# Performance work log

Hardware: AMD Instinct MI355X
Metric: run time of the kernel (lower is better)

Reference implementation:

```python
import jax, jax.numpy as jnp
import numpy as np

MAX_P = 20
MAX_N = 50
FDIM = 256
SCALE = 0.08
STEPS = 3


def _grid_sample_border(feat_hwc, grid):
    # feat_hwc: [B,H,W,C]; grid: [B,Q,2] normalized xy in [-1,1]
    # Bilinear grid_sample, padding_mode='border', align_corners=False (matches torch).
    B, H, W, C = feat_hwc.shape

    def one(fm, g):  # fm [H,W,C], g [Q,2]
        ix = jnp.clip(((g[:, 0] + 1.0) * W - 1.0) * 0.5, 0.0, W - 1.0)
        iy = jnp.clip(((g[:, 1] + 1.0) * H - 1.0) * 0.5, 0.0, H - 1.0)
        x0f = jnp.floor(ix); y0f = jnp.floor(iy)
        wx = (ix - x0f)[:, None]; wy = (iy - y0f)[:, None]
        x0 = x0f.astype(jnp.int32); y0 = y0f.astype(jnp.int32)
        x1 = jnp.minimum(x0 + 1, W - 1); y1 = jnp.minimum(y0 + 1, H - 1)
        f00 = fm[y0, x0]; f01 = fm[y0, x1]  # [Q,C]
        f10 = fm[y1, x0]; f11 = fm[y1, x1]
        top = f00 * (1.0 - wx) + f01 * wx
        bot = f10 * (1.0 - wx) + f11 * wx
        return top * (1.0 - wy) + bot * wy

    return jax.vmap(one)(feat_hwc, grid)


def setup_inputs() -> dict:
    key = jax.random.key(0)
    ks = jax.random.split(key, 12)
    d = {
        'p2': jax.random.normal(ks[0], (4, 256, 256, 256), jnp.float32),
        'p4': jax.random.normal(ks[1], (4, 256, 64, 64), jnp.float32),
        'iw1': jax.random.normal(ks[2], (16384, 512), jnp.float32) * 0.01,
        'ib1': jnp.zeros((512,), jnp.float32),
        'iw2': jax.random.normal(ks[3], (512, 1024), jnp.float32) * 0.04,
        'ib2': jnp.zeros((1024,), jnp.float32),
        'iw3': jax.random.normal(ks[4], (1024, 2000), jnp.float32) * 0.03,
        'ib3': jnp.zeros((2000,), jnp.float32),
        'rw1': jax.random.normal(ks[5], (258, 256), jnp.float32) * 0.06,
        'rb1': jnp.zeros((256,), jnp.float32),
        'rw2': jax.random.normal(ks[6], (256, 128), jnp.float32) * 0.06,
        'rb2': jnp.zeros((128,), jnp.float32),
        'rw3': jax.random.normal(ks[7], (128, 2), jnp.float32) * 0.09,
        'rb3': jnp.zeros((2,), jnp.float32),
        'vw1': jax.random.normal(ks[8], (100, 128), jnp.float32) * 0.1,
        'vb1': jnp.zeros((128,), jnp.float32),
        'vw2': jax.random.normal(ks[9], (128, 1), jnp.float32) * 0.09,
        'vb2': jnp.zeros((1,), jnp.float32),
    }
    return d


def reference(p2, p4, iw1, ib1, iw2, ib2, iw3, ib3,
              rw1, rb1, rw2, rb2, rw3, rb3, vw1, vb1, vw2, vb2):
    B = p4.shape[0]
    # AdaptiveAvgPool2d(8) on 64x64 -> mean over 8x8 blocks
    pooled = p4.reshape(B, FDIM, 8, 8, 8, 8).mean(axis=(3, 5))  # [B,C,8,8]
    flat = pooled.reshape(B, -1)  # [B, C*64]
    h = jax.nn.relu(flat @ iw1 + ib1)
    h = jax.nn.relu(h @ iw2 + ib2)
    init_polygons = jax.nn.sigmoid(h @ iw3 + ib3).reshape(B, MAX_P, MAX_N, 2)

    feat_hwc = jnp.transpose(p2, (0, 2, 3, 1))  # [B,H,W,C]
    polygons = init_polygons
    for _ in range(STEPS):
        coords = polygons.reshape(B, -1, 2)           # [B,Q,2] in [0,1]
        grid = coords * 2.0 - 1.0
        sampled = _grid_sample_border(feat_hwc, grid)  # [B,Q,C]
        inp = jnp.concatenate([sampled, coords], axis=-1)  # [B,Q,C+2]
        r = jax.nn.relu(inp @ rw1 + rb1)
        r = jax.nn.relu(r @ rw2 + rb2)
        disp = jnp.tanh(r @ rw3 + rb3).reshape(B, MAX_P, MAX_N, 2)
        bad = ~jnp.all(jnp.isfinite(disp))
        disp = jnp.where(bad, 0.0,
                         jnp.clip(disp * SCALE, -2.0 * SCALE, 2.0 * SCALE))
        polygons = jnp.clip(polygons + disp, 0.0, 1.0)

    poly_flat = polygons.reshape(B * MAX_P, MAX_N * 2)
    v = jax.nn.relu(poly_flat @ vw1 + vb1)
    validity = jax.nn.sigmoid(v @ vw2 + vb2).reshape(B, MAX_P)
    return polygons, validity, init_polygons
```

## Files before the change

### kernel.cpp

```cpp
#include <hip/hip_runtime.h>
#include <hip/hip_fp16.h>
#include <math.h>

#define WS_FLAT 0
#define WS_PART 65536
#define WS_H1   (65536 + 524288)
#define WS_H2   (WS_H1 + 2048)
#define WS_POLY (WS_H2 + 4096)
#define WS_P2T  1048576

__global__ void __launch_bounds__(256) transpose_k(const float* __restrict__ in,
                                                   __half* __restrict__ out) {
    __shared__ float t[64][65];
    int tile = blockIdx.x;
    int b  = tile >> 12;
    int ct = (tile >> 10) & 3;
    int xt = tile & 1023;
    int c0 = ct << 6, yx0 = xt << 6;
    int tid = threadIdx.x;

    int jv = (tid & 15) << 2;
    int i0 = tid >> 4;
    const float* ip = in + (((size_t)(b * 256 + c0)) << 16) + yx0;
    #pragma unroll
    for (int ii = i0; ii < 64; ii += 16) {
        float4 v = *(const float4*)(ip + ((size_t)ii << 16) + jv);
        t[jv + 0][ii] = v.x; t[jv + 1][ii] = v.y;
        t[jv + 2][ii] = v.z; t[jv + 3][ii] = v.w;
    }
    __syncthreads();

    int cl = (tid & 7) << 3;
    #pragma unroll
    for (int jj = tid >> 3; jj < 64; jj += 32) {
        union { __half h[8]; float4 f; } u;
        #pragma unroll
        for (int q = 0; q < 8; ++q) u.h[q] = __float2half(t[jj][cl + q]);
        *(float4*)(out + ((size_t)b << 24) + ((size_t)(yx0 + jj) << 8) + c0 + cl) = u.f;
    }
}

__global__ void pool_k(const float* __restrict__ p4, float* __restrict__ flat) {
    int o = blockIdx.x * blockDim.x + threadIdx.x;
    int b = o >> 14;
    int c = (o >> 6) & 255;
    int ij = o & 63;
    int i = ij >> 3, j = ij & 7;
    const float* base = p4 + (((size_t)(b * 256 + c) * 64 + i * 8) * 64 + j * 8);
    float s = 0.f;
    #pragma unroll
    for (int u = 0; u < 8; ++u) {
        const float4* r = (const float4*)(base + u * 64);
        float4 a = r[0], bb = r[1];
        s += a.x + a.y + a.z + a.w + bb.x + bb.y + bb.z + bb.w;
    }
    flat[o] = s * (1.0f / 64.0f);
}

__global__ void g1a_k(const float* __restrict__ flat, const float* __restrict__ iw1,
                      float* __restrict__ part) {
    __shared__ float sf[4][64];
    int tid = threadIdx.x;
    int kbase = blockIdx.x * 64;
    if (tid < 256) sf[tid >> 6][tid & 63] = flat[(tid >> 6) * 16384 + kbase + (tid & 63)];
    __syncthreads();
    float a0 = 0.f, a1 = 0.f, a2 = 0.f, a3 = 0.f;
    for (int k = 0; k < 64; ++k) {
        float w = iw1[(size_t)(kbase + k) * 512 + tid];
        a0 = fmaf(sf[0][k], w, a0);
        a1 = fmaf(sf[1][k], w, a1);
        a2 = fmaf(sf[2][k], w, a2);
        a3 = fmaf(sf[3][k], w, a3);
    }
    float* pp = part + (size_t)blockIdx.x * 2048;
    pp[tid] = a0; pp[512 + tid] = a1; pp[1024 + tid] = a2; pp[1536 + tid] = a3;
}

__global__ void g1b_k(const float* __restrict__ part, const float* __restrict__ ib1,
                      float* __restrict__ h1) {
    __shared__ float red[8][32];
    int tid = threadIdx.x;
    int cc = tid >> 5, oo = tid & 31;
    int o = blockIdx.x * 32 + oo;
    float s = 0.f;
    for (int i = 0; i < 32; ++i)
        s += part[(size_t)(cc + 8 * i) * 2048 + o];
    red[cc][oo] = s;
    __syncthreads();
    if (cc == 0) {
        float t = 0.f;
        #pragma unroll
        for (int c2 = 0; c2 < 8; ++c2) t += red[c2][oo];
        t += ib1[o & 511];
        h1[o] = fmaxf(t, 0.f);
    }
}

__global__ void g2_k(const float* __restrict__ h1, const float* __restrict__ iw2,
                     const float* __restrict__ ib2, float* __restrict__ h2) {
    __shared__ float sh[512];
    __shared__ float red[4][64];
    int tid = threadIdx.x;
    int b = blockIdx.x >> 4, jt = blockIdx.x & 15;
    sh[tid] = h1[b * 512 + tid];
    sh[tid + 256] = h1[b * 512 + 256 + tid];
    __syncthreads();
    int j = (jt << 6) + (tid & 63);
    int kc = tid >> 6;
    float acc = 0.f;
    for (int k = kc * 128; k < kc * 128 + 128; ++k)
        acc = fmaf(sh[k], iw2[(size_t)k * 1024 + j], acc);
    red[kc][tid & 63] = acc;
    __syncthreads();
    if (kc == 0) {
        float t = red[0][tid] + red[1][tid] + red[2][tid] + red[3][tid] + ib2[j];
        h2[b * 1024 + j] = fmaxf(t, 0.f);
    }
}

__global__ void g3_k(const float* __restrict__ h2, const float* __restrict__ iw3,
                     const float* __restrict__ ib3, float* __restrict__ out_init,
                     float* __restrict__ poly) {
    __shared__ float sh[1024];
    __shared__ float red[4][64];
    int tid = threadIdx.x;
    int b = blockIdx.x >> 5, jt = blockIdx.x & 31;
    const float* h = h2 + b * 1024;
    sh[tid] = h[tid]; sh[tid + 256] = h[tid + 256];
    sh[tid + 512] = h[tid + 512]; sh[tid + 768] = h[tid + 768];
    __syncthreads();
    int j = (jt << 6) + (tid & 63);
    int kc = tid >> 6;
    float acc = 0.f;
    if (j < 2000) {
        for (int k = kc * 256; k < kc * 256 + 256; ++k)
            acc = fmaf(sh[k], iw3[(size_t)k * 2000 + j], acc);
    }
    red[kc][tid & 63] = acc;
    __syncthreads();
    if (kc == 0 && j < 2000) {
        float t = red[0][tid] + red[1][tid] + red[2][tid] + red[3][tid] + ib3[j];
        float s = 1.f / (1.f + expf(-t));
        int o = b * 2000 + j;
        out_init[o] = s;
        poly[o] = s;
    }
}

__global__ void __launch_bounds__(256) step_k(
    const __half* __restrict__ p2th,
    const float* __restrict__ rw1, const float* __restrict__ rb1,
    const float* __restrict__ rw2, const float* __restrict__ rb2,
    const float* __restrict__ rw3, const float* __restrict__ rb3,
    float* __restrict__ poly) {
    __shared__ __align__(16) float s_inp[258 * 16];
    __shared__ __align__(16) float s_r1[256 * 16];
    __shared__ __align__(16) float s_r2[128 * 16];
    int tid = threadIdx.x;
    int pt0 = blockIdx.x * 16;

    {
        int ch2 = (tid & 127) << 1;
        int pgg = tid >> 7;
        float v0[8], v1[8];
        #pragma unroll
        for (int pp = 0; pp < 8; ++pp) {
            int pt = pt0 + pgg * 8 + pp;
            int b = pt / 1000;
            float cx = poly[pt * 2], cy = poly[pt * 2 + 1];
            float ix = fminf(fmaxf(cx * 256.f - 0.5f, 0.f), 255.f);
            float iy = fminf(fmaxf(cy * 256.f - 0.5f, 0.f), 255.f);
            float x0f = floorf(ix), y0f = floorf(iy);
            int x0 = (int)x0f, y0 = (int)y0f;
            int x1 = min(x0 + 1, 255), y1 = min(y0 + 1, 255);
            float wx = ix - x0f, wy = iy - y0f;
            const __half* bt = p2th + ((size_t)b << 24);
            int r0 = (y0 << 16) + (x0 << 8) + ch2;
            int r1a = (y1 << 16) + (x0 << 8) + ch2;
            int dx = (x1 - x0) << 8;
            float2 f00 = __half22float2(*(const __half2*)(bt + r0));
            float2 f01 = __half22float2(*(const __half2*)(bt + r0 + dx));
            float2 f10 = __half22float2(*(const __half2*)(bt + r1a));
            float2 f11 = __half22float2(*(const __half2*)(bt + r1a + dx));
            float t0 = f00.x + (f01.x - f00.x) * wx;
            float b0 = f10.x + (f11.x - f10.x) * wx;
            float t1 = f00.y + (f01.y - f00.y) * wx;
            float b1 = f10.y + (f11.y - f10.y) * wx;
            v0[pp] = t0 + (b0 - t0) * wy;
            v1[pp] = t1 + (b1 - t1) * wy;
        }
        float* r0p = &s_inp[ch2 * 16 + pgg * 8];
        float* r1p = &s_inp[(ch2 + 1) * 16 + pgg * 8];
        ((float4*)r0p)[0] = make_float4(v0[0], v0[1], v0[2], v0[3]);
        ((float4*)r0p)[1] = make_float4(v0[4], v0[5], v0[6], v0[7]);
        ((float4*)r1p)[0] = make_float4(v1[0], v1[1], v1[2], v1[3]);
        ((float4*)r1p)[1] = make_float4(v1[4], v1[5], v1[6], v1[7]);
        if (tid < 32) {
            int p = tid >> 1, d = tid & 1;
            s_inp[(256 + d) * 16 + p] = poly[(pt0 + p) * 2 + d];
        }
    }
    __syncthreads();

    int jc = tid & 63, pg = tid >> 6;
    {
        float4 bias = *(const float4*)(rb1 + jc * 4);
        float4 acc0 = bias, acc1 = bias, acc2 = bias, acc3 = bias;
        for (int k = 0; k < 258; ++k) {
            float4 a = *(const float4*)&s_inp[k * 16 + pg * 4];
            float4 w = *(const float4*)(rw1 + k * 256 + jc * 4);
            acc0.x = fmaf(a.x, w.x, acc0.x); acc0.y = fmaf(a.x, w.y, acc0.y);
            acc0.z = fmaf(a.x, w.z, acc0.z); acc0.w = fmaf(a.x, w.w, acc0.w);
            acc1.x = fmaf(a.y, w.x, acc1.x); acc1.y = fmaf(a.y, w.y, acc1.y);
            acc1.z = fmaf(a.y, w.z, acc1.z); acc1.w = fmaf(a.y, w.w, acc1.w);
            acc2.x = fmaf(a.z, w.x, acc2.x); acc2.y = fmaf(a.z, w.y, acc2.y);
            acc2.z = fmaf(a.z, w.z, acc2.z); acc2.w = fmaf(a.z, w.w, acc2.w);
            acc3.x = fmaf(a.w, w.x, acc3.x); acc3.y = fmaf(a.w, w.y, acc3.y);
            acc3.z = fmaf(a.w, w.z, acc3.z); acc3.w = fmaf(a.w, w.w, acc3.w);
        }
        acc0.x = fmaxf(acc0.x, 0.f); acc0.y = fmaxf(acc0.y, 0.f);
        acc0.z = fmaxf(acc0.z, 0.f); acc0.w = fmaxf(acc0.w, 0.f);
        acc1.x = fmaxf(acc1.x, 0.f); acc1.y = fmaxf(acc1.y, 0.f);
        acc1.z = fmaxf(acc1.z, 0.f); acc1.w = fmaxf(acc1.w, 0.f);
        acc2.x = fmaxf(acc2.x, 0.f); acc2.y = fmaxf(acc2.y, 0.f);
        acc2.z = fmaxf(acc2.z, 0.f); acc2.w = fmaxf(acc2.w, 0.f);
        acc3.x = fmaxf(acc3.x, 0.f); acc3.y = fmaxf(acc3.y, 0.f);
        acc3.z = fmaxf(acc3.z, 0.f); acc3.w = fmaxf(acc3.w, 0.f);
        *(float4*)&s_r1[(jc * 4 + 0) * 16 + pg * 4] = make_float4(acc0.x, acc1.x, acc2.x, acc3.x);
        *(float4*)&s_r1[(jc * 4 + 1) * 16 + pg * 4] = make_float4(acc0.y, acc1.y, acc2.y, acc3.y);
        *(float4*)&s_r1[(jc * 4 + 2) * 16 + pg * 4] = make_float4(acc0.z, acc1.z, acc2.z, acc3.z);
        *(float4*)&s_r1[(jc * 4 + 3) * 16 + pg * 4] = make_float4(acc0.w, acc1.w, acc2.w, acc3.w);
    }
    __syncthreads();

    {
        float2 bias = *(const float2*)(rb2 + jc * 2);
        float2 d0 = bias, d1 = bias, d2 = bias, d3 = bias;
        for (int k = 0; k < 256; ++k) {
            float4 a = *(const float4*)&s_r1[k * 16 + pg * 4];
            float2 w = *(const float2*)(rw2 + k * 128 + jc * 2);
            d0.x = fmaf(a.x, w.x, d0.x); d0.y = fmaf(a.x, w.y, d0.y);
            d1.x = fmaf(a.y, w.x, d1.x); d1.y = fmaf(a.y, w.y, d1.y);
            d2.x = fmaf(a.z, w.x, d2.x); d2.y = fmaf(a.z, w.y, d2.y);
            d3.x = fmaf(a.w, w.x, d3.x); d3.y = fmaf(a.w, w.y, d3.y);
        }
        d0.x = fmaxf(d0.x, 0.f); d0.y = fmaxf(d0.y, 0.f);
        d1.x = fmaxf(d1.x, 0.f); d1.y = fmaxf(d1.y, 0.f);
        d2.x = fmaxf(d2.x, 0.f); d2.y = fmaxf(d2.y, 0.f);
        d3.x = fmaxf(d3.x, 0.f); d3.y = fmaxf(d3.y, 0.f);
        *(float4*)&s_r2[(jc * 2 + 0) * 16 + pg * 4] = make_float4(d0.x, d1.x, d2.x, d3.x);
        *(float4*)&s_r2[(jc * 2 + 1) * 16 + pg * 4] = make_float4(d0.y, d1.y, d2.y, d3.y);
    }
    __syncthreads();

    if (tid < 32) {
        int p = tid >> 1, d = tid & 1;
        float acc = rb3[d];
        for (int k = 0; k < 128; ++k)
            acc = fmaf(s_r2[k * 16 + p], rw3[k * 2 + d], acc);
        float disp = tanhf(acc) * 0.08f;
        disp = fminf(fmaxf(disp, -0.16f), 0.16f);
        int idx = (pt0 + p) * 2 + d;
        float nv = poly[idx] + disp;
        poly[idx] = fminf(fmaxf(nv, 0.f), 1.f);
    }
}

__global__ void valid_k(const float* __restrict__ poly,
                        const float* __restrict__ vw1, const float* __restrict__ vb1,
                        const float* __restrict__ vw2, const float* __restrict__ vb2,
                        float* __restrict__ out) {
    __shared__ float sp[100];
    __shared__ float sred[2];
    int tid = threadIdx.x;
    int row = blockIdx.x;
    if (tid < 100) {
        float v = poly[row * 100 + tid];
        sp[tid] = v;
        out[row * 100 + tid] = v;
    }
    __syncthreads();
    float acc = vb1[tid];
    for (int k = 0; k < 100; ++k)
        acc = fmaf(sp[k], vw1[k * 128 + tid], acc);
    float pr = fmaxf(acc, 0.f) * vw2[tid];
    #pragma unroll
    for (int off = 32; off > 0; off >>= 1)
        pr += __shfl_down(pr, off, 64);
    if ((tid & 63) == 0) sred[tid >> 6] = pr;
    __syncthreads();
    if (tid == 0) {
        float s = sred[0] + sred[1] + vb2[0];
        out[8000 + row] = 1.f / (1.f + expf(-s));
    }
}

extern "C" void kernel_launch(void* const* d_in, const int* in_sizes, int n_in,
                              void* d_out, int out_size, void* d_ws, size_t ws_size,
                              hipStream_t stream) {
    const float* p2  = (const float*)d_in[0];
    const float* p4  = (const float*)d_in[1];
    const float* iw1 = (const float*)d_in[2];
    const float* ib1 = (const float*)d_in[3];
    const float* iw2 = (const float*)d_in[4];
    const float* ib2 = (const float*)d_in[5];
    const float* iw3 = (const float*)d_in[6];
    const float* ib3 = (const float*)d_in[7];
    const float* rw1 = (const float*)d_in[8];
    const float* rb1 = (const float*)d_in[9];
    const float* rw2 = (const float*)d_in[10];
    const float* rb2 = (const float*)d_in[11];
    const float* rw3 = (const float*)d_in[12];
    const float* rb3 = (const float*)d_in[13];
    const float* vw1 = (const float*)d_in[14];
    const float* vb1 = (const float*)d_in[15];
    const float* vw2 = (const float*)d_in[16];
    const float* vb2 = (const float*)d_in[17];
    float* out = (float*)d_out;
    float* ws = (float*)d_ws;
    float* flat = ws + WS_FLAT;
    float* part = ws + WS_PART;
    float* h1   = ws + WS_H1;
    float* h2   = ws + WS_H2;
    float* poly = ws + WS_POLY;
    __half* p2th = (__half*)(ws + WS_P2T);

    pool_k<<<256, 256, 0, stream>>>(p4, flat);
    g1a_k<<<256, 512, 0, stream>>>(flat, iw1, part);
    g1b_k<<<64, 256, 0, stream>>>(part, ib1, h1);
    g2_k<<<64, 256, 0, stream>>>(h1, iw2, ib2, h2);
    g3_k<<<128, 256, 0, stream>>>(h2, iw3, ib3, out + 8080, poly);
    transpose_k<<<16384, 256, 0, stream>>>(p2, p2th);
    for (int s = 0; s < 3; ++s)
        step_k<<<250, 256, 0, stream>>>(p2th, rw1, rb1, rw2, rb2, rw3, rb3, poly);
    valid_k<<<80, 128, 0, stream>>>(poly, vw1, vb1, vw2, vb2, out);
}
```

Baseline: 584.1 us.

## Fuse pooling, first GEMV and p2 transpose into one kernel; halve step block size

Merges the p4 pooling into the first MLP partial-GEMV kernel, and packs that with the p2 NCHW→NHWC fp16 transpose into a single 512-thread launch partitioned by block index. This removes launches and lets the small MLP work overlap the bandwidth-bound transpose. The refine step kernel now handles 8 points per block instead of 16, giving 500 blocks for better CU coverage. In exchange each block re-reads the weights per point pair, so weight traffic doubles, and shared memory moves to a row-major layout.

Result: slower. 599.2 us (+2.6%).

```diff
diff --git a/kernel.cpp b/kernel.cpp
--- a/kernel.cpp
+++ b/kernel.cpp
@@ -9,71 +9,64 @@
 #define WS_POLY (WS_H2 + 4096)
 #define WS_P2T  1048576
 
-__global__ void __launch_bounds__(256) transpose_k(const float* __restrict__ in,
-                                                   __half* __restrict__ out) {
-    __shared__ float t[64][65];
-    int tile = blockIdx.x;
-    int b  = tile >> 12;
-    int ct = (tile >> 10) & 3;
-    int xt = tile & 1023;
-    int c0 = ct << 6, yx0 = xt << 6;
-    int tid = threadIdx.x;
-
-    int jv = (tid & 15) << 2;
-    int i0 = tid >> 4;
-    const float* ip = in + (((size_t)(b * 256 + c0)) << 16) + yx0;
-    #pragma unroll
-    for (int ii = i0; ii < 64; ii += 16) {
-        float4 v = *(const float4*)(ip + ((size_t)ii << 16) + jv);
-        t[jv + 0][ii] = v.x; t[jv + 1][ii] = v.y;
-        t[jv + 2][ii] = v.z; t[jv + 3][ii] = v.w;
-    }
-    __syncthreads();
-
-    int cl = (tid & 7) << 3;
-    #pragma unroll
-    for (int jj = tid >> 3; jj < 64; jj += 32) {
+__global__ void __launch_bounds__(512) fused_tp_g1a(
+    const float* __restrict__ p2, __half* __restrict__ p2th,
+    const float* __restrict__ p4, const float* __restrict__ iw1,
+    float* __restrict__ part) {
+    __shared__ float smem[64 * 65];
+    int tid = threadIdx.x;
+
+    if (blockIdx.x < 256) {
+        int kb = blockIdx.x;
+        float* sf = smem;
+        if (tid < 256) {
+            int b = tid >> 6, ij = tid & 63;
+            const float* base = p4 + (((size_t)(b * 256 + kb) * 64 + (ij >> 3) * 8) * 64 + (ij & 7) * 8);
+            float s = 0.f;
+            #pragma unroll
+            for (int u = 0; u < 8; ++u) {
+                const float4* r = (const float4*)(base + u * 64);
+                float4 a = r[0], bb = r[1];
+                s += a.x + a.y + a.z + a.w + bb.x + bb.y + bb.z + bb.w;
+            }
+            sf[tid] = s * (1.0f / 64.0f);
+        }
+        __syncthreads();
+        float a0 = 0.f, a1 = 0.f, a2 = 0.f, a3 = 0.f;
+        int kbase = kb << 6;
+        for (int k = 0; k < 64; ++k) {
+            float w = iw1[(size_t)(kbase + k) * 512 + tid];
+            a0 = fmaf(sf[k],       w, a0);
+            a1 = fmaf(sf[64 + k],  w, a1);
+            a2 = fmaf(sf[128 + k], w, a2);
+            a3 = fmaf(sf[192 + k], w, a3);
+        }
+        float* pp = part + (size_t)kb * 2048;
+        pp[tid] = a0; pp[512 + tid] = a1; pp[1024 + tid] = a2; pp[1536 + tid] = a3;
+    } else {
+        int tile = blockIdx.x - 256;
+        int b  = tile >> 12;
+        int ct = (tile >> 10) & 3;
+        int xt = tile & 1023;
+        int c0 = ct << 6, yx0 = xt << 6;
+        float (*t)[65] = (float (*)[65])smem;
+
+        int jv = (tid & 15) << 2;
+        const float* ip = p2 + (((size_t)(b * 256 + c0)) << 16) + yx0;
+        #pragma unroll
+        for (int ii = tid >> 4; ii < 64; ii += 32) {
+            float4 v = *(const float4*)(ip + ((size_t)ii << 16) + jv);
+            t[jv + 0][ii] = v.x; t[jv + 1][ii] = v.y;
+            t[jv + 2][ii] = v.z; t[jv + 3][ii] = v.w;
+        }
+        __syncthreads();
+        int cl = (tid & 7) << 3;
+        int jj = tid >> 3;
         union { __half h[8]; float4 f; } u;
         #pragma unroll
         for (int q = 0; q < 8; ++q) u.h[q] = __float2half(t[jj][cl + q]);
-        *(float4*)(out + ((size_t)b << 24) + ((size_t)(yx0 + jj) << 8) + c0 + cl) = u.f;
-    }
-}
-
-__global__ void pool_k(const float* __restrict__ p4, float* __restrict__ flat) {
-    int o = blockIdx.x * blockDim.x + threadIdx.x;
-    int b = o >> 14;
-    int c = (o >> 6) & 255;
-    int ij = o & 63;
-    int i = ij >> 3, j = ij & 7;
-    const float* base = p4 + (((size_t)(b * 256 + c) * 64 + i * 8) * 64 + j * 8);
-    float s = 0.f;
-    #pragma unroll
-    for (int u = 0; u < 8; ++u) {
-        const float4* r = (const float4*)(base + u * 64);
-        float4 a = r[0], bb = r[1];
-        s += a.x + a.y + a.z + a.w + bb.x + bb.y + bb.z + bb.w;
-    }
-    flat[o] = s * (1.0f / 64.0f);
-}
-
-__global__ void g1a_k(const float* __restrict__ flat, const float* __restrict__ iw1,
-                      float* __restrict__ part) {
-    __shared__ float sf[4][64];
-    int tid = threadIdx.x;
-    int kbase = blockIdx.x * 64;
-    if (tid < 256) sf[tid >> 6][tid & 63] = flat[(tid >> 6) * 16384 + kbase + (tid & 63)];
-    __syncthreads();
-    float a0 = 0.f, a1 = 0.f, a2 = 0.f, a3 = 0.f;
-    for (int k = 0; k < 64; ++k) {
-        float w = iw1[(size_t)(kbase + k) * 512 + tid];
-        a0 = fmaf(sf[0][k], w, a0);
-        a1 = fmaf(sf[1][k], w, a1);
-        a2 = fmaf(sf[2][k], w, a2);
-        a3 = fmaf(sf[3][k], w, a3);
-    }
-    float* pp = part + (size_t)blockIdx.x * 2048;
-    pp[tid] = a0; pp[512 + tid] = a1; pp[1024 + tid] = a2; pp[1536 + tid] = a3;
+        *(float4*)(p2th + ((size_t)b << 24) + ((size_t)(yx0 + jj) << 8) + c0 + cl) = u.f;
+    }
 }
 
 __global__ void g1b_k(const float* __restrict__ part, const float* __restrict__ ib1,
@@ -153,23 +146,23 @@
     const float* __restrict__ rw2, const float* __restrict__ rb2,
     const float* __restrict__ rw3, const float* __restrict__ rb3,
     float* __restrict__ poly) {
-    __shared__ __align__(16) float s_inp[258 * 16];
-    __shared__ __align__(16) float s_r1[256 * 16];
-    __shared__ __align__(16) float s_r2[128 * 16];
-    int tid = threadIdx.x;
-    int pt0 = blockIdx.x * 16;
+    __shared__ __align__(16) float s_inp[8][258];
+    __shared__ __align__(16) float s_r1[8][256];
+    __shared__ __align__(16) float s_r2[8][130];
+    int tid = threadIdx.x;
+    int pt0 = blockIdx.x * 8;
 
     {
         int ch2 = (tid & 127) << 1;
         int pgg = tid >> 7;
-        float v0[8], v1[8];
         #pragma unroll
-        for (int pp = 0; pp < 8; ++pp) {
-            int pt = pt0 + pgg * 8 + pp;
+        for (int pp = 0; pp < 4; ++pp) {
+            int lp = pgg * 4 + pp;
+            int pt = pt0 + lp;
             int b = pt / 1000;
-            float cx = poly[pt * 2], cy = poly[pt * 2 + 1];
-            float ix = fminf(fmaxf(cx * 256.f - 0.5f, 0.f), 255.f);
-            float iy = fminf(fmaxf(cy * 256.f - 0.5f, 0.f), 255.f);
+            float2 cxy = *(const float2*)(poly + pt * 2);
+            float ix = fminf(fmaxf(cxy.x * 256.f - 0.5f, 0.f), 255.f);
+            float iy = fminf(fmaxf(cxy.y * 256.f - 0.5f, 0.f), 255.f);
             float x0f = floorf(ix), y0f = floorf(iy);
             int x0 = (int)x0f, y0 = (int)y0f;
             int x1 = min(x0 + 1, 255), y1 = min(y0 + 1, 255);
@@ -186,18 +179,12 @@
             float b0 = f10.x + (f11.x - f10.x) * wx;
             float t1 = f00.y + (f01.y - f00.y) * wx;
             float b1 = f10.y + (f11.y - f10.y) * wx;
-            v0[pp] = t0 + (b0 - t0) * wy;
-            v1[pp] = t1 + (b1 - t1) * wy;
-        }
-        float* r0p = &s_inp[ch2 * 16 + pgg * 8];
-        float* r1p = &s_inp[(ch2 + 1) * 16 + pgg * 8];
-        ((float4*)r0p)[0] = make_float4(v0[0], v0[1], v0[2], v0[3]);
-        ((float4*)r0p)[1] = make_float4(v0[4], v0[5], v0[6], v0[7]);
-        ((float4*)r1p)[0] = make_float4(v1[0], v1[1], v1[2], v1[3]);
-        ((float4*)r1p)[1] = make_float4(v1[4], v1[5], v1[6], v1[7]);
-        if (tid < 32) {
+            *(float2*)&s_inp[lp][ch2] = make_float2(t0 + (b0 - t0) * wy,
+                                                    t1 + (b1 - t1) * wy);
+        }
+        if (tid < 16) {
             int p = tid >> 1, d = tid & 1;
-            s_inp[(256 + d) * 16 + p] = poly[(pt0 + p) * 2 + d];
+            s_inp[p][256 + d] = poly[(pt0 + p) * 2 + d];
         }
     }
     __syncthreads();
@@ -205,59 +192,49 @@
     int jc = tid & 63, pg = tid >> 6;
     {
         float4 bias = *(const float4*)(rb1 + jc * 4);
-        float4 acc0 = bias, acc1 = bias, acc2 = bias, acc3 = bias;
+        float4 acc0 = bias, acc1 = bias;
+        const float* r0 = s_inp[pg * 2];
+        const float* r1 = s_inp[pg * 2 + 1];
         for (int k = 0; k < 258; ++k) {
-            float4 a = *(const float4*)&s_inp[k * 16 + pg * 4];
             float4 w = *(const float4*)(rw1 + k * 256 + jc * 4);
-            acc0.x = fmaf(a.x, w.x, acc0.x); acc0.y = fmaf(a.x, w.y, acc0.y);
-            acc0.z = fmaf(a.x, w.z, acc0.z); acc0.w = fmaf(a.x, w.w, acc0.w);
-            acc1.x = fmaf(a.y, w.x, acc1.x); acc1.y = fmaf(a.y, w.y, acc1.y);
-            acc1.z = fmaf(a.y, w.z, acc1.z); acc1.w = fmaf(a.y, w.w, acc1.w);
-            acc2.x = fmaf(a.z, w.x, acc2.x); acc2.y = fmaf(a.z, w.y, acc2.y);
-            acc2.z = fmaf(a.z, w.z, acc2.z); acc2.w = fmaf(a.z, w.w, acc2.w);
-            acc3.x = fmaf(a.w, w.x, acc3.x); acc3.y = fmaf(a.w, w.y, acc3.y);
-            acc3.z = fmaf(a.w, w.z, acc3.z); acc3.w = fmaf(a.w, w.w, acc3.w);
+            float a0 = r0[k], a1 = r1[k];
+            acc0.x = fmaf(a0, w.x, acc0.x); acc0.y = fmaf(a0, w.y, acc0.y);
+            acc0.z = fmaf(a0, w.z, acc0.z); acc0.w = fmaf(a0, w.w, acc0.w);
+            acc1.x = fmaf(a1, w.x, acc1.x); acc1.y = fmaf(a1, w.y, acc1.y);
+            acc1.z = fmaf(a1, w.z, acc1.z); acc1.w = fmaf(a1, w.w, acc1.w);
         }
         acc0.x = fmaxf(acc0.x, 0.f); acc0.y = fmaxf(acc0.y, 0.f);
         acc0.z = fmaxf(acc0.z, 0.f); acc0.w = fmaxf(acc0.w, 0.f);
         acc1.x = fmaxf(acc1.x, 0.f); acc1.y = fmaxf(acc1.y, 0.f);
         acc1.z = fmaxf(acc1.z, 0.f); acc1.w = fmaxf(acc1.w, 0.f);
-        acc2.x = fmaxf(acc2.x, 0.f); acc2.y = fmaxf(acc2.y, 0.f);
-        acc2.z = fmaxf(acc2.z, 0.f); acc2.w = fmaxf(acc2.w, 0.f);
-        acc3.x = fmaxf(acc3.x, 0.f); acc3.y = fmaxf(acc3.y, 0.f);
-        acc3.z = fmaxf(acc3.z, 0.f); acc3.w = fmaxf(acc3.w, 0.f);
-        *(float4*)&s_r1[(jc * 4 + 0) * 16 + pg * 4] = make_float4(acc0.x, acc1.x, acc2.x, acc3.x);
-        *(float4*)&s_r1[(jc * 4 + 1) * 16 + pg * 4] = make_float4(acc0.y, acc1.y, acc2.y, acc3.y);
-        *(float4*)&s_r1[(jc * 4 + 2) * 16 + pg * 4] = make_float4(acc0.z, acc1.z, acc2.z, acc3.z);
-        *(float4*)&s_r1[(jc * 4 + 3) * 16 + pg * 4] = make_float4(acc0.w, acc1.w, acc2.w, acc3.w);
+        *(float4*)&s_r1[pg * 2][jc * 4] = acc0;
+        *(float4*)&s_r1[pg * 2 + 1][jc * 4] = acc1;
     }
     __syncthreads();
 
     {
         float2 bias = *(const float2*)(rb2 + jc * 2);
-        float2 d0 = bias, d1 = bias, d2 = bias, d3 = bias;
+        float2 d0 = bias, d1 = bias;
+        const float* r0 = s_r1[pg * 2];
+        const float* r1 = s_r1[pg * 2 + 1];
         for (int k = 0; k < 256; ++k) {
-            float4 a = *(const float4*)&s_r1[k * 16 + pg * 4];
             float2 w = *(const float2*)(rw2 + k * 128 + jc * 2);
-            d0.x = fmaf(a.x, w.x, d0.x); d0.y = fmaf(a.x, w.y, d0.y);
-            d1.x = fmaf(a.y, w.x, d1.x); d1.y = fmaf(a.y, w.y, d1.y);
-            d2.x = fmaf(a.z, w.x, d2.x); d2.y = fmaf(a.z, w.y, d2.y);
-            d3.x = fmaf(a.w, w.x, d3.x); d3.y = fmaf(a.w, w.y, d3.y);
+            float a0 = r0[k], a1 = r1[k];
+            d0.x = fmaf(a0, w.x, d0.x); d0.y = fmaf(a0, w.y, d0.y);
+            d1.x = fmaf(a1, w.x, d1.x); d1.y = fmaf(a1, w.y, d1.y);
         }
         d0.x = fmaxf(d0.x, 0.f); d0.y = fmaxf(d0.y, 0.f);
         d1.x = fmaxf(d1.x, 0.f); d1.y = fmaxf(d1.y, 0.f);
-        d2.x = fmaxf(d2.x, 0.f); d2.y = fmaxf(d2.y, 0.f);
-        d3.x = fmaxf(d3.x, 0.f); d3.y = fmaxf(d3.y, 0.f);
-        *(float4*)&s_r2[(jc * 2 + 0) * 16 + pg * 4] = make_float4(d0.x, d1.x, d2.x, d3.x);
-        *(float4*)&s_r2[(jc * 2 + 1) * 16 + pg * 4] = make_float4(d0.y, d1.y, d2.y, d3.y);
-    }
-    __syncthreads();
-
-    if (tid < 32) {
+        *(float2*)&s_r2[pg * 2][jc * 2] = d0;
+        *(float2*)&s_r2[pg * 2 + 1][jc * 2] = d1;
+    }
+    __syncthreads();
+
+    if (tid < 16) {
         int p = tid >> 1, d = tid & 1;
         float acc = rb3[d];
         for (int k = 0; k < 128; ++k)
-            acc = fmaf(s_r2[k * 16 + p], rw3[k * 2 + d], acc);
+            acc = fmaf(s_r2[p][k], rw3[k * 2 + d], acc);
         float disp = tanhf(acc) * 0.08f;
         disp = fminf(fmaxf(disp, -0.16f), 0.16f);
         int idx = (pt0 + p) * 2 + d;
@@ -318,20 +295,17 @@
     const float* vb2 = (const float*)d_in[17];
     float* out = (float*)d_out;
     float* ws = (float*)d_ws;
-    float* flat = ws + WS_FLAT;
     float* part = ws + WS_PART;
     float* h1   = ws + WS_H1;
     float* h2   = ws + WS_H2;
     float* poly = ws + WS_POLY;
     __half* p2th = (__half*)(ws + WS_P2T);
 
-    pool_k<<<256, 256, 0, stream>>>(p4, flat);
-    g1a_k<<<256, 512, 0, stream>>>(flat, iw1, part);
+    fused_tp_g1a<<<16640, 512, 0, stream>>>(p2, p2th, p4, iw1, part);
     g1b_k<<<64, 256, 0, stream>>>(part, ib1, h1);
     g2_k<<<64, 256, 0, stream>>>(h1, iw2, ib2, h2);
     g3_k<<<128, 256, 0, stream>>>(h2, iw3, ib3, out + 8080, poly);
-    transpose_k<<<16384, 256, 0, stream>>>(p2, p2th);
     for (int s = 0; s < 3; ++s)
-        step_k<<<250, 256, 0, stream>>>(p2th, rw1, rb1, rw2, rb2, rw3, rb3, poly);
+        step_k<<<500, 256, 0, stream>>>(p2th, rw1, rb1, rw2, rb2, rw3, rb3, poly);
     valid_k<<<80, 128, 0, stream>>>(poly, vw1, vb1, vw2, vb2, out);
 }
```

## Fuse pooling, MLP head and p2 transpose into one kernel with last-block reduction

Applied to the files above, without the earlier changes.

Replaces six separate launches (pool, three GEMV stages, transpose) with one kernel. The first 256 blocks compute pooling plus layer-1 partial sums. The last block to finish, found with an atomic counter, runs the final reduction and layers 2 and 3 serially. The remaining blocks transpose p2 to fp16 with 512 threads each, so the small MLP overlaps the bandwidth-bound transpose and launch overhead goes away. The risk is that one block now does the whole iw2/iw3 GEMV (about 10 MB of weights) alone, which could become a long serial tail, and a memset launch is added to reset the counter.

Result: slower. 824.6 us (+41.2%).

```diff
diff --git a/kernel.cpp b/kernel.cpp
--- a/kernel.cpp
+++ b/kernel.cpp
@@ -2,148 +2,146 @@
 #include <hip/hip_fp16.h>
 #include <math.h>
 
-#define WS_FLAT 0
+#define WS_CNT  0
 #define WS_PART 65536
-#define WS_H1   (65536 + 524288)
-#define WS_H2   (WS_H1 + 2048)
-#define WS_POLY (WS_H2 + 4096)
+#define WS_POLY (65536 + 524288)
 #define WS_P2T  1048576
 
-__global__ void __launch_bounds__(256) transpose_k(const float* __restrict__ in,
-                                                   __half* __restrict__ out) {
-    __shared__ float t[64][65];
-    int tile = blockIdx.x;
-    int b  = tile >> 12;
-    int ct = (tile >> 10) & 3;
-    int xt = tile & 1023;
-    int c0 = ct << 6, yx0 = xt << 6;
+__global__ void __launch_bounds__(512) fused_tp_g1a(
+    const float* __restrict__ p2, __half* __restrict__ p2th,
+    const float* __restrict__ p4, const float* __restrict__ iw1,
+    const float* __restrict__ ib1,
+    const float* __restrict__ iw2, const float* __restrict__ ib2,
+    const float* __restrict__ iw3, const float* __restrict__ ib3,
+    float* __restrict__ part, int* __restrict__ cnt,
+    float* __restrict__ out_init, float* __restrict__ poly) {
+    __shared__ __align__(16) float smem[6144];
+    __shared__ int isLast;
     int tid = threadIdx.x;
 
-    int jv = (tid & 15) << 2;
-    int i0 = tid >> 4;
-    const float* ip = in + (((size_t)(b * 256 + c0)) << 16) + yx0;
-    #pragma unroll
-    for (int ii = i0; ii < 64; ii += 16) {
-        float4 v = *(const float4*)(ip + ((size_t)ii << 16) + jv);
-        t[jv + 0][ii] = v.x; t[jv + 1][ii] = v.y;
-        t[jv + 2][ii] = v.z; t[jv + 3][ii] = v.w;
-    }
-    __syncthreads();
-
-    int cl = (tid & 7) << 3;
-    #pragma unroll
-    for (int jj = tid >> 3; jj < 64; jj += 32) {
+    if (blockIdx.x < 256) {
+        int kb = blockIdx.x;
+        float* sf = smem;
+        if (tid < 256) {
+            int b = tid >> 6, ij = tid & 63;
+            const float* base = p4 + (((size_t)(b * 256 + kb) * 64 + (ij >> 3) * 8) * 64 + (ij & 7) * 8);
+            float s = 0.f;
+            #pragma unroll
+            for (int u = 0; u < 8; ++u) {
+                const float4* r = (const float4*)(base + u * 64);
+                float4 a = r[0], bb = r[1];
+                s += a.x + a.y + a.z + a.w + bb.x + bb.y + bb.z + bb.w;
+            }
+            sf[tid] = s * (1.0f / 64.0f);
+        }
+        __syncthreads();
+        float a0 = 0.f, a1 = 0.f, a2 = 0.f, a3 = 0.f;
+        int kbase = kb << 6;
+        for (int k = 0; k < 64; ++k) {
+            float w = iw1[(size_t)(kbase + k) * 512 + tid];
+            a0 = fmaf(sf[k],       w, a0);
+            a1 = fmaf(sf[64 + k],  w, a1);
+            a2 = fmaf(sf[128 + k], w, a2);
+            a3 = fmaf(sf[192 + k], w, a3);
+        }
+        float* pp = part + (size_t)kb * 2048;
+        pp[tid] = a0; pp[512 + tid] = a1; pp[1024 + tid] = a2; pp[1536 + tid] = a3;
+
+        __threadfence();
+        __syncthreads();
+        if (tid == 0) {
+            int old = atomicAdd(cnt, 1);
+            isLast = (old == 255);
+        }
+        __syncthreads();
+        if (!isLast) return;
+        __threadfence();
+
+        float* h1s = smem;
+        float* h2s = smem + 2048;
+        {
+            int o0 = tid * 4;
+            float4 acc = make_float4(0.f, 0.f, 0.f, 0.f);
+            for (int k2 = 0; k2 < 256; ++k2) {
+                float4 p = *(const float4*)&part[(size_t)k2 * 2048 + o0];
+                acc.x += p.x; acc.y += p.y; acc.z += p.z; acc.w += p.w;
+            }
+            float4 bb = *(const float4*)&ib1[o0 & 511];
+            h1s[o0 + 0] = fmaxf(acc.x + bb.x, 0.f);
+            h1s[o0 + 1] = fmaxf(acc.y + bb.y, 0.f);
+            h1s[o0 + 2] = fmaxf(acc.z + bb.z, 0.f);
+            h1s[o0 + 3] = fmaxf(acc.w + bb.w, 0.f);
+        }
+        __syncthreads();
+        {
+            int j0 = tid * 2;
+            float2 bb = *(const float2*)&ib2[j0];
+            float2 a0v = bb, a1v = bb, a2v = bb, a3v = bb;
+            for (int k = 0; k < 512; ++k) {
+                float2 w = *(const float2*)&iw2[(size_t)k * 1024 + j0];
+                float h0 = h1s[k], h1v = h1s[512 + k], h2v = h1s[1024 + k], h3 = h1s[1536 + k];
+                a0v.x = fmaf(h0, w.x, a0v.x); a0v.y = fmaf(h0, w.y, a0v.y);
+                a1v.x = fmaf(h1v, w.x, a1v.x); a1v.y = fmaf(h1v, w.y, a1v.y);
+                a2v.x = fmaf(h2v, w.x, a2v.x); a2v.y = fmaf(h2v, w.y, a2v.y);
+                a3v.x = fmaf(h3, w.x, a3v.x); a3v.y = fmaf(h3, w.y, a3v.y);
+            }
+            __syncthreads();
+            h2s[j0] = fmaxf(a0v.x, 0.f); h2s[j0 + 1] = fmaxf(a0v.y, 0.f);
+            h2s[1024 + j0] = fmaxf(a1v.x, 0.f); h2s[1024 + j0 + 1] = fmaxf(a1v.y, 0.f);
+            h2s[2048 + j0] = fmaxf(a2v.x, 0.f); h2s[2048 + j0 + 1] = fmaxf(a2v.y, 0.f);
+            h2s[3072 + j0] = fmaxf(a3v.x, 0.f); h2s[3072 + j0 + 1] = fmaxf(a3v.y, 0.f);
+        }
+        __syncthreads();
+        if (tid < 500) {
+            int j0 = tid * 4;
+            float4 bb = *(const float4*)&ib3[j0];
+            float4 acc[4] = {bb, bb, bb, bb};
+            for (int k = 0; k < 1024; ++k) {
+                float4 w = *(const float4*)&iw3[(size_t)k * 2000 + j0];
+                #pragma unroll
+                for (int b = 0; b < 4; ++b) {
+                    float hv = h2s[b * 1024 + k];
+                    acc[b].x = fmaf(hv, w.x, acc[b].x);
+                    acc[b].y = fmaf(hv, w.y, acc[b].y);
+                    acc[b].z = fmaf(hv, w.z, acc[b].z);
+                    acc[b].w = fmaf(hv, w.w, acc[b].w);
+                }
+            }
+            #pragma unroll
+            for (int b = 0; b < 4; ++b) {
+                float4 s;
+                s.x = 1.f / (1.f + expf(-acc[b].x));
+                s.y = 1.f / (1.f + expf(-acc[b].y));
+                s.z = 1.f / (1.f + expf(-acc[b].z));
+                s.w = 1.f / (1.f + expf(-acc[b].w));
+                int o = b * 2000 + j0;
+                *(float4*)&out_init[o] = s;
+                *(float4*)&poly[o] = s;
+            }
+        }
+    } else {
+        int tile = blockIdx.x - 256;
+        int b  = tile >> 12;
+        int ct = (tile >> 10) & 3;
+        int xt = tile & 1023;
+        int c0 = ct << 6, yx0 = xt << 6;
+        float (*t)[65] = (float (*)[65])smem;
+
+        int jv = (tid & 15) << 2;
+        const float* ip = p2 + (((size_t)(b * 256 + c0)) << 16) + yx0;
+        #pragma unroll
+        for (int ii = tid >> 4; ii < 64; ii += 32) {
+            float4 v = *(const float4*)(ip + ((size_t)ii << 16) + jv);
+            t[jv + 0][ii] = v.x; t[jv + 1][ii] = v.y;
+            t[jv + 2][ii] = v.z; t[jv + 3][ii] = v.w;
+        }
+        __syncthreads();
+        int cl = (tid & 7) << 3;
+        int jj = tid >> 3;
         union { __half h[8]; float4 f; } u;
         #pragma unroll
         for (int q = 0; q < 8; ++q) u.h[q] = __float2half(t[jj][cl + q]);
-        *(float4*)(out + ((size_t)b << 24) + ((size_t)(yx0 + jj) << 8) + c0 + cl) = u.f;
-    }
-}
-
-__global__ void pool_k(const float* __restrict__ p4, float* __restrict__ flat) {
-    int o = blockIdx.x * blockDim.x + threadIdx.x;
-    int b = o >> 14;
-    int c = (o >> 6) & 255;
-    int ij = o & 63;
-    int i = ij >> 3, j = ij & 7;
-    const float* base = p4 + (((size_t)(b * 256 + c) * 64 + i * 8) * 64 + j * 8);
-    float s = 0.f;
-    #pragma unroll
-    for (int u = 0; u < 8; ++u) {
-        const float4* r = (const float4*)(base + u * 64);
-        float4 a = r[0], bb = r[1];
-        s += a.x + a.y + a.z + a.w + bb.x + bb.y + bb.z + bb.w;
-    }
-    flat[o] = s * (1.0f / 64.0f);
-}
-
-__global__ void g1a_k(const float* __restrict__ flat, const float* __restrict__ iw1,
-                      float* __restrict__ part) {
-    __shared__ float sf[4][64];
-    int tid = threadIdx.x;
-    int kbase = blockIdx.x * 64;
-    if (tid < 256) sf[tid >> 6][tid & 63] = flat[(tid >> 6) * 16384 + kbase + (tid & 63)];
-    __syncthreads();
-    float a0 = 0.f, a1 = 0.f, a2 = 0.f, a3 = 0.f;
-    for (int k = 0; k < 64; ++k) {
-        float w = iw1[(size_t)(kbase + k) * 512 + tid];
-        a0 = fmaf(sf[0][k], w, a0);
-        a1 = fmaf(sf[1][k], w, a1);
-        a2 = fmaf(sf[2][k], w, a2);
-        a3 = fmaf(sf[3][k], w, a3);
-    }
-    float* pp = part + (size_t)blockIdx.x * 2048;
-    pp[tid] = a0; pp[512 + tid] = a1; pp[1024 + tid] = a2; pp[1536 + tid] = a3;
-}
-
-__global__ void g1b_k(const float* __restrict__ part, const float* __restrict__ ib1,
-                      float* __restrict__ h1) {
-    __shared__ float red[8][32];
-    int tid = threadIdx.x;
-    int cc = tid >> 5, oo = tid & 31;
-    int o = blockIdx.x * 32 + oo;
-    float s = 0.f;
-    for (int i = 0; i < 32; ++i)
-        s += part[(size_t)(cc + 8 * i) * 2048 + o];
-    red[cc][oo] = s;
-    __syncthreads();
-    if (cc == 0) {
-        float t = 0.f;
-        #pragma unroll
-        for (int c2 = 0; c2 < 8; ++c2) t += red[c2][oo];
-        t += ib1[o & 511];
-        h1[o] = fmaxf(t, 0.f);
-    }
-}
-
-__global__ void g2_k(const float* __restrict__ h1, const float* __restrict__ iw2,
-                     const float* __restrict__ ib2, float* __restrict__ h2) {
-    __shared__ float sh[512];
-    __shared__ float red[4][64];
-    int tid = threadIdx.x;
-    int b = blockIdx.x >> 4, jt = blockIdx.x & 15;
-    sh[tid] = h1[b * 512 + tid];
-    sh[tid + 256] = h1[b * 512 + 256 + tid];
-    __syncthreads();
-    int j = (jt << 6) + (tid & 63);
-    int kc = tid >> 6;
-    float acc = 0.f;
-    for (int k = kc * 128; k < kc * 128 + 128; ++k)
-        acc = fmaf(sh[k], iw2[(size_t)k * 1024 + j], acc);
-    red[kc][tid & 63] = acc;
-    __syncthreads();
-    if (kc == 0) {
-        float t = red[0][tid] + red[1][tid] + red[2][tid] + red[3][tid] + ib2[j];
-        h2[b * 1024 + j] = fmaxf(t, 0.f);
-    }
-}
-
-__global__ void g3_k(const float* __restrict__ h2, const float* __restrict__ iw3,
-                     const float* __restrict__ ib3, float* __restrict__ out_init,
-                     float* __restrict__ poly) {
-    __shared__ float sh[1024];
-    __shared__ float red[4][64];
-    int tid = threadIdx.x;
-    int b = blockIdx.x >> 5, jt = blockIdx.x & 31;
-    const float* h = h2 + b * 1024;
-    sh[tid] = h[tid]; sh[tid + 256] = h[tid + 256];
-    sh[tid + 512] = h[tid + 512]; sh[tid + 768] = h[tid + 768];
-    __syncthreads();
-    int j = (jt << 6) + (tid & 63);
-    int kc = tid >> 6;
-    float acc = 0.f;
-    if (j < 2000) {
-        for (int k = kc * 256; k < kc * 256 + 256; ++k)
-            acc = fmaf(sh[k], iw3[(size_t)k * 2000 + j], acc);
-    }
-    red[kc][tid & 63] = acc;
-    __syncthreads();
-    if (kc == 0 && j < 2000) {
-        float t = red[0][tid] + red[1][tid] + red[2][tid] + red[3][tid] + ib3[j];
-        float s = 1.f / (1.f + expf(-t));
-        int o = b * 2000 + j;
-        out_init[o] = s;
-        poly[o] = s;
+        *(float4*)(p2th + ((size_t)b << 24) + ((size_t)(yx0 + jj) << 8) + c0 + cl) = u.f;
     }
 }
 
@@ -318,19 +316,14 @@
     const float* vb2 = (const float*)d_in[17];
     float* out = (float*)d_out;
     float* ws = (float*)d_ws;
-    float* flat = ws + WS_FLAT;
     float* part = ws + WS_PART;
-    float* h1   = ws + WS_H1;
-    float* h2   = ws + WS_H2;
     float* poly = ws + WS_POLY;
+    int*   cnt  = (int*)(ws + WS_CNT);
     __half* p2th = (__half*)(ws + WS_P2T);
 
-    pool_k<<<256, 256, 0, stream>>>(p4, flat);
-    g1a_k<<<256, 512, 0, stream>>>(flat, iw1, part);
-    g1b_k<<<64, 256, 0, stream>>>(part, ib1, h1);
-    g2_k<<<64, 256, 0, stream>>>(h1, iw2, ib2, h2);
-    g3_k<<<128, 256, 0, stream>>>(h2, iw3, ib3, out + 8080, poly);
-    transpose_k<<<16384, 256, 0, stream>>>(p2, p2th);
+    hipMemsetAsync(cnt, 0, sizeof(int), stream);
+    fused_tp_g1a<<<16640, 512, 0, stream>>>(p2, p2th, p4, iw1, ib1, iw2, ib2,
+                                            iw3, ib3, part, cnt, out + 8080, poly);
     for (int s = 0; s < 3; ++s)
         step_k<<<250, 256, 0, stream>>>(p2th, rw1, rb1, rw2, rb2, rw3, rb3, poly);
     valid_k<<<80, 128, 0, stream>>>(poly, vw1, vb1, vw2, vb2, out);
```
